# Optimization experiments

Hardware: AMD Instinct MI355X
Metric: run time of the kernel (lower is better)

## Reference

```python
import jax, jax.numpy as jnp
import numpy as np

NUM_HEADS = 16
DIM = 1024
HEAD_DIM = DIM // NUM_HEADS
SCALE = HEAD_DIM ** -0.5


def setup_inputs() -> dict:
    key = jax.random.key(0)
    ks = jax.random.split(key, 6)
    b, n = 2, 1024
    x = jax.random.normal(ks[0], (b, n, DIM), dtype=jnp.float32)
    Wq = jax.random.normal(ks[1], (DIM, DIM), dtype=jnp.float32) * 0.02
    bq = jnp.zeros((DIM,), dtype=jnp.float32)
    Wkv = jax.random.normal(ks[2], (2 * DIM, DIM), dtype=jnp.float32) * 0.02
    bkv = jnp.zeros((2 * DIM,), dtype=jnp.float32)
    Wp = jax.random.normal(ks[3], (DIM, DIM), dtype=jnp.float32) * 0.02
    bp = jnp.zeros((DIM,), dtype=jnp.float32)
    return {"x": x, "Wq": Wq, "bq": bq, "Wkv": Wkv, "bkv": bkv, "Wp": Wp, "bp": bp}


def reference(x, Wq, bq, Wkv, bkv, Wp, bp):
    b, n, c = x.shape
    h, dh = NUM_HEADS, HEAD_DIM
    # self-attention: y = x
    q = (x @ Wq.T + bq).reshape(b, n, h, dh)              # bnhd
    kv = (x @ Wkv.T + bkv).reshape(b, n, 2, h, dh)
    k, v = kv[:, :, 0], kv[:, :, 1]                       # bmhd each
    attn = jnp.einsum('bnhd,bmhd->bnmh', q, k) * SCALE    # bnmh scores
    attn = jax.nn.softmax(attn, axis=2)                   # softmax over m
    out = jnp.einsum('bnmh,bmhd->bnhd', attn, v).reshape(b, n, c)
    out = out @ Wp.T + bp
    return (out, attn)
```

## Files before the change

kernel.cpp:

```cpp
#include <hip/hip_runtime.h>
#include <hip/hip_bf16.h>
#include <stdint.h>


#define NB   2
#define SEQ  1024
#define CDIM 1024
#define NH   16
#define HD   64
#define ROWS (NB*SEQ)
#define ATT_SCALE 0.125f

typedef __attribute__((ext_vector_type(8))) short bf16x8;
typedef __attribute__((ext_vector_type(4))) float f32x4;

#define MFMA16(a,b,c) __builtin_amdgcn_mfma_f32_16x16x32_bf16((a),(b),(c),0,0,0)

static __device__ __forceinline__ unsigned short f2bf(float f) {
  uint32_t x = __builtin_bit_cast(uint32_t, f);
  return (unsigned short)((x + 0x7fffu + ((x >> 16) & 1u)) >> 16);
}
static __device__ __forceinline__ float bf2f(unsigned short u) {
  uint32_t x = ((uint32_t)u) << 16;
  return __builtin_bit_cast(float, x);
}

static __device__ __forceinline__ void gl_lds16(const unsigned short* g,
                                                unsigned short* l) {
  __builtin_amdgcn_global_load_lds(
      (const __attribute__((address_space(1))) unsigned int*)g,
      (__attribute__((address_space(3))) unsigned int*)l,
      16, 0, 0);
}

__global__ __launch_bounds__(256) void k_convert(
    const float* __restrict__ x, const float* __restrict__ Wq,
    const float* __restrict__ Wkv, const float* __restrict__ Wp,
    unsigned short* __restrict__ Xhi, unsigned short* __restrict__ Xlo,
    unsigned short* __restrict__ Whi, unsigned short* __restrict__ Wlo)
{
  const int NX = ROWS * CDIM;
  const int NW = 4096 * CDIM;
  int i = blockIdx.x * 256 + threadIdx.x;
  if (i < NX) {
    float f = x[i];
    unsigned short h = f2bf(f);
    Xhi[i] = h; Xlo[i] = f2bf(f - bf2f(h));
  } else if (i < NX + NW) {
    int w = i - NX;
    int j = w >> 10, c = w & 1023;
    float f = (j < 1024) ? Wq[(size_t)j*1024 + c]
            : (j < 3072) ? Wkv[(size_t)(j-1024)*1024 + c]
                         : Wp[(size_t)(j-3072)*1024 + c];
    unsigned short h = f2bf(f);
    Whi[w] = h; Wlo[w] = f2bf(f - bf2f(h));
  }
}

struct EpiQKV {
  const float* bq; const float* bkv;
  unsigned short *Qhi, *Qlo, *Khi, *Klo, *Vthi, *Vtlo;
  __device__ __forceinline__ void operator()(int m, int n, float v) const {
    if (n < 1024) {
      v += bq[n];
      unsigned short h = f2bf(v);
      size_t o = (size_t)m*1024 + n;
      Qhi[o] = h; Qlo[o] = f2bf(v - bf2f(h));
    } else if (n < 2048) {
      v += bkv[n - 1024];
      size_t o = (size_t)m*1024 + (n - 1024);
      unsigned short h = f2bf(v);
      Khi[o] = h; Klo[o] = f2bf(v - bf2f(h));
    } else {
      v += bkv[n - 1024];
      int c = n - 2048;
      int hh = c >> 6, d = c & 63;
      int b = m >> 10, mm = m & 1023;
      size_t o = ((size_t)((b*NH + hh)*HD + d))*SEQ + mm;
      unsigned short h = f2bf(v);
      Vthi[o] = h; Vtlo[o] = f2bf(v - bf2f(h));
    }
  }
};
struct EpiOut {
  const float* bp; float* out;
  __device__ __forceinline__ void operator()(int m, int n, float v) const {
    out[(size_t)m*1024 + n] = v + bp[n];
  }
};

template <int BM, int BN, class Epi>
__device__ __forceinline__ void gemm_core(
    const unsigned short* __restrict__ Ahi, const unsigned short* __restrict__ Alo, int lda,
    const unsigned short* __restrict__ Bhi, const unsigned short* __restrict__ Blo, int ldb,
    int K, const Epi& epi)
{
  constexpr int FM = BM/32, FN = BN/32;
  constexpr int CA = BM/16, CB = BN/16;
  constexpr int TOT = 2*(CA+CB);
  __shared__ unsigned short sAh[BM*32], sAl[BM*32], sBh[BN*32], sBl[BN*32];
  const int tid  = threadIdx.x;
  const int lane = tid & 63, wave = tid >> 6;
  const int wm = wave & 1, wn = wave >> 1;
  const int bn = blockIdx.x * BN, bm = blockIdx.y * BM;
  const int r = lane & 15, q = lane >> 4;
  const int crow = lane >> 2, ccol = (lane & 3) * 8;

  f32x4 acc[FM][FN];
  #pragma unroll
  for (int i = 0; i < FM; i++)
    #pragma unroll
    for (int j = 0; j < FN; j++) {
      acc[i][j][0]=0.f; acc[i][j][1]=0.f; acc[i][j][2]=0.f; acc[i][j][3]=0.f;
    }

  for (int k0 = 0; k0 < K; k0 += 32) {
    #pragma unroll
    for (int t = 0; t < TOT/4; t++) {
      int c = wave + t*4;
      const unsigned short* gb; unsigned short* sb; int rr, grow, ld;
      if (c < CA)            { gb=Ahi; sb=sAh; rr=c;         grow=bm; ld=lda; }
      else if (c < 2*CA)     { gb=Alo; sb=sAl; rr=c-CA;      grow=bm; ld=lda; }
      else if (c < 2*CA+CB)  { gb=Bhi; sb=sBh; rr=c-2*CA;    grow=bn; ld=ldb; }
      else                   { gb=Blo; sb=sBl; rr=c-2*CA-CB; grow=bn; ld=ldb; }
      int row = rr*16 + crow;
      gl_lds16(gb + (size_t)(grow + row)*ld + k0 + ccol, sb + rr*512);
    }
    __syncthreads();
    bf16x8 ah[FM], al[FM], bh[FN], bl[FN];
    #pragma unroll
    for (int i = 0; i < FM; i++) {
      int oa = (wm*(BM/2) + i*16 + r)*32 + q*8;
      ah[i] = *(const bf16x8*)(sAh + oa);
      al[i] = *(const bf16x8*)(sAl + oa);
    }
    #pragma unroll
    for (int j = 0; j < FN; j++) {
      int ob = (wn*(BN/2) + j*16 + r)*32 + q*8;
      bh[j] = *(const bf16x8*)(sBh + ob);
      bl[j] = *(const bf16x8*)(sBl + ob);
    }
    #pragma unroll
    for (int i = 0; i < FM; i++)
      #pragma unroll
      for (int j = 0; j < FN; j++) {
        acc[i][j] = MFMA16(ah[i], bh[j], acc[i][j]);
        acc[i][j] = MFMA16(ah[i], bl[j], acc[i][j]);
        acc[i][j] = MFMA16(al[i], bh[j], acc[i][j]);
      }
    __syncthreads();
  }
  #pragma unroll
  for (int i = 0; i < FM; i++)
    #pragma unroll
    for (int j = 0; j < FN; j++)
      #pragma unroll
      for (int t = 0; t < 4; t++)
        epi(bm + wm*(BM/2) + i*16 + q*4 + t, bn + wn*(BN/2) + j*16 + r, acc[i][j][t]);
}

__global__ __launch_bounds__(256) void k_gemm_qkv(
    const unsigned short* Xhi, const unsigned short* Xlo,
    const unsigned short* Whi, const unsigned short* Wlo,
    const float* bq, const float* bkv,
    unsigned short* Qhi, unsigned short* Qlo,
    unsigned short* Khi, unsigned short* Klo,
    unsigned short* Vthi, unsigned short* Vtlo)
{
  EpiQKV e{bq, bkv, Qhi, Qlo, Khi, Klo, Vthi, Vtlo};
  gemm_core<128,128>(Xhi, Xlo, CDIM, Whi, Wlo, CDIM, CDIM, e);
}

__global__ __launch_bounds__(256) void k_gemm_out(
    const unsigned short* OAhi, const unsigned short* OAlo,
    const unsigned short* Wphi, const unsigned short* Wplo,
    const float* bp, float* out)
{
  EpiOut e{bp, out};
  gemm_core<64,64>(OAhi, OAlo, CDIM, Wphi, Wplo, CDIM, CDIM, e);
}

#define SLAB_PAD 20
__global__ __launch_bounds__(128) void k_logits(
    const unsigned short* __restrict__ Qhi, const unsigned short* __restrict__ Qlo,
    const unsigned short* __restrict__ Khi, const unsigned short* __restrict__ Klo,
    float* __restrict__ attn)
{
  int mt = blockIdx.x, nt = blockIdx.y, b = blockIdx.z;
  int n0 = nt*16, m0 = mt*32;
  __shared__ unsigned short sQh[16*64], sQl[16*64], sKh[32*64], sKl[32*64];
  __shared__ float slab[16*32*SLAB_PAD];
  const int tid = threadIdx.x, lane = tid & 63, wave = tid >> 6;
  const int r = lane & 15, q = lane >> 4;
  const int crow8 = lane >> 3, ccol8 = (lane & 7) * 8;

  for (int h = 0; h < NH; h++) {
    #pragma unroll
    for (int t = 0; t < 6; t++) {
      int c = wave + t*2;
      const unsigned short* gb; unsigned short* sb; int rr, base;
      if (c < 2)      { gb=Qhi; sb=sQh; rr=c;   base=n0; }
      else if (c < 4) { gb=Qlo; sb=sQl; rr=c-2; base=n0; }
      else if (c < 8) { gb=Khi; sb=sKh; rr=c-4; base=m0; }
      else            { gb=Klo; sb=sKl; rr=c-8; base=m0; }
      int row = rr*8 + crow8;
      gl_lds16(gb + (size_t)(b*SEQ + base + row)*CDIM + h*HD + ccol8, sb + rr*512);
    }
    __syncthreads();
    {
      f32x4 acc; acc[0]=0.f; acc[1]=0.f; acc[2]=0.f; acc[3]=0.f;
      #pragma unroll
      for (int ks = 0; ks < 2; ks++) {
        bf16x8 qh = *(const bf16x8*)(sQh + r*64 + ks*32 + q*8);
        bf16x8 ql = *(const bf16x8*)(sQl + r*64 + ks*32 + q*8);
        bf16x8 kh = *(const bf16x8*)(sKh + (wave*16 + r)*64 + ks*32 + q*8);
        bf16x8 kl = *(const bf16x8*)(sKl + (wave*16 + r)*64 + ks*32 + q*8);
        acc = MFMA16(qh, kh, acc);
        acc = MFMA16(qh, kl, acc);
        acc = MFMA16(ql, kh, acc);
      }
      #pragma unroll
      for (int t = 0; t < 4; t++) {
        int nn = q*4 + t;
        int mm = wave*16 + r;
        slab[(nn*32 + mm)*SLAB_PAD + h] = acc[t] * ATT_SCALE;
      }
    }
    __syncthreads();
  }
  for (int it = 0; it < 16; it++) {
    int idx = it*128 + tid;
    int nn = idx >> 7;
    int rem = idx & 127;
    int flat = rem * 4;
    int mm = flat >> 4, hh = flat & 15;
    float4 v = *(float4*)&slab[(nn*32 + mm)*SLAB_PAD + hh];
    size_t g = (size_t)(b*SEQ + n0 + nn)*(SEQ*NH) + (size_t)(m0 + mm)*NH + hh;
    *(float4*)(attn + g) = v;
  }
}

__global__ __launch_bounds__(256) void k_softmax(
    float* __restrict__ attn, unsigned short* __restrict__ P,
    float* __restrict__ scale_pv)
{
  int n = blockIdx.x, b = blockIdx.y;
  __shared__ float slab[SEQ*NH];
  __shared__ float red[256];
  __shared__ float gmax[16], ginv[16];
  const int tid = threadIdx.x;
  const size_t base = (size_t)(b*SEQ + n) * (SEQ*NH);

  for (int it = 0; it < 16; it++) {
    int f4 = it*256 + tid;
    *(float4*)&slab[f4*4] = *(const float4*)(attn + base + (size_t)f4*4);
  }
  __syncthreads();
  const int h = tid & 15, mq = tid >> 4;
  float mx = -1e30f;
  for (int i = 0; i < 64; i++) mx = fmaxf(mx, slab[(mq*64 + i)*16 + h]);
  red[tid] = mx;
  __syncthreads();
  if (tid < 16) {
    float m2 = red[tid];
    for (int j = 1; j < 16; j++) m2 = fmaxf(m2, red[j*16 + tid]);
    gmax[tid] = m2;
  }
  __syncthreads();
  float gm = gmax[h];
  float s = 0.f;
  for (int i = 0; i < 64; i++) {
    int idx = (mq*64 + i)*16 + h;
    float p = __expf(slab[idx] - gm);
    slab[idx] = p;
    s += p;
  }
  red[tid] = s;
  __syncthreads();
  if (tid < 16) {
    float s2 = 0.f;
    for (int j = 0; j < 16; j++) s2 += red[j*16 + tid];
    float inv = 1.0f / s2;
    ginv[tid] = inv;
    scale_pv[(size_t)(b*SEQ + n)*NH + tid] = inv * (1.0f/65535.0f);
  }
  __syncthreads();
  for (int it = 0; it < 16; it++) {
    int f4 = it*256 + tid;
    int flat = f4*4;
    int hh = flat & 15;
    float4 v = *(float4*)&slab[flat];
    float4 iv = *(float4*)&ginv[hh];
    v.x *= iv.x; v.y *= iv.y; v.z *= iv.z; v.w *= iv.w;
    *(float4*)(attn + base + (size_t)flat) = v;
  }
  int h2 = tid >> 4, l16 = tid & 15;
  size_t pbase = ((size_t)((b*NH + h2)*SEQ + n))*SEQ;
  for (int i = 0; i < 64; i++) {
    int m = i*16 + l16;
    float p = slab[m*16 + h2];
    unsigned int u = (unsigned int)(p * 65535.0f + 0.5f);
    P[pbase + m] = (unsigned short)u;
  }
}

__global__ __launch_bounds__(256) void k_pv(
    const unsigned short* __restrict__ P,
    const unsigned short* __restrict__ Vthi, const unsigned short* __restrict__ Vtlo,
    const float* __restrict__ scale_pv,
    unsigned short* __restrict__ OAhi, unsigned short* __restrict__ OAlo)
{
  int nt = blockIdx.x, h = blockIdx.y, b = blockIdx.z;
  int n0 = nt * 64;
  __shared__ unsigned short sPa[64*32], sPb[64*32], sVh[64*32], sVl[64*32];
  const int tid = threadIdx.x, lane = tid & 63, wave = tid >> 6;
  const int wm = wave & 1, wn = wave >> 1;
  const int r = lane & 15, q = lane >> 4;
  const int crow = lane >> 2, ccol = (lane & 3) * 8;
  const size_t pbase = ((size_t)(b*NH + h))*SEQ*SEQ;
  const size_t vbase = ((size_t)(b*NH + h))*HD*SEQ;

  f32x4 acc[2][2];
  #pragma unroll
  for (int i = 0; i < 2; i++)
    #pragma unroll
    for (int j = 0; j < 2; j++) {
      acc[i][j][0]=0.f; acc[i][j][1]=0.f; acc[i][j][2]=0.f; acc[i][j][3]=0.f;
    }

  for (int k0 = 0; k0 < SEQ; k0 += 32) {
    #pragma unroll
    for (int t = 0; t < 2; t++) {
      int c = wave + t*4;
      const unsigned short* gb = (c < 4) ? Vthi : Vtlo;
      unsigned short* sb = (c < 4) ? (unsigned short*)sVh : (unsigned short*)sVl;
      int rr = c & 3;
      int row = rr*16 + crow;
      gl_lds16(gb + vbase + (size_t)row*SEQ + k0 + ccol, sb + rr*512);
    }
    {
      int row = tid >> 2, ch = (tid & 3) * 8;
      uint4 v = *(const uint4*)(P + pbase + (size_t)(n0 + row)*SEQ + k0 + ch);
      unsigned int wds[4] = {v.x, v.y, v.z, v.w};
      unsigned int pa[4], pb[4];
      #pragma unroll
      for (int e = 0; e < 4; e++) {
        unsigned int lo16 = wds[e] & 0xFFFFu;
        unsigned int hi16 = wds[e] >> 16;
        unsigned int a0 = __builtin_bit_cast(uint32_t, (float)(lo16 & 0xFF00u)) >> 16;
        unsigned int b0 = __builtin_bit_cast(uint32_t, (float)(lo16 & 0x00FFu)) >> 16;
        unsigned int a1 = __builtin_bit_cast(uint32_t, (float)(hi16 & 0xFF00u)) >> 16;
        unsigned int b1 = __builtin_bit_cast(uint32_t, (float)(hi16 & 0x00FFu)) >> 16;
        pa[e] = a0 | (a1 << 16);
        pb[e] = b0 | (b1 << 16);
      }
      *(uint4*)(sPa + row*32 + ch) = make_uint4(pa[0],pa[1],pa[2],pa[3]);
      *(uint4*)(sPb + row*32 + ch) = make_uint4(pb[0],pb[1],pb[2],pb[3]);
    }
    __syncthreads();
    bf16x8 pa[2], pb[2], vh[2], vl[2];
    #pragma unroll
    for (int i = 0; i < 2; i++) {
      int off = (wm*32 + i*16 + r)*32 + q*8;
      pa[i] = *(const bf16x8*)(sPa + off);
      pb[i] = *(const bf16x8*)(sPb + off);
    }
    #pragma unroll
    for (int j = 0; j < 2; j++) {
      int off = (wn*32 + j*16 + r)*32 + q*8;
      vh[j] = *(const bf16x8*)(sVh + off);
      vl[j] = *(const bf16x8*)(sVl + off);
    }
    #pragma unroll
    for (int i = 0; i < 2; i++)
      #pragma unroll
      for (int j = 0; j < 2; j++) {
        acc[i][j] = MFMA16(pa[i], vh[j], acc[i][j]);
        acc[i][j] = MFMA16(pb[i], vh[j], acc[i][j]);
        acc[i][j] = MFMA16(pa[i], vl[j], acc[i][j]);
      }
    __syncthreads();
  }
  #pragma unroll
  for (int i = 0; i < 2; i++)
    #pragma unroll
    for (int t = 0; t < 4; t++) {
      int nn = n0 + wm*32 + i*16 + q*4 + t;
      float sc = scale_pv[(size_t)(b*SEQ + nn)*NH + h];
      #pragma unroll
      for (int j = 0; j < 2; j++) {
        int d = wn*32 + j*16 + r;
        float val = acc[i][j][t] * sc;
        size_t o = (size_t)(b*SEQ + nn)*CDIM + h*HD + d;
        unsigned short hb = f2bf(val);
        OAhi[o] = hb; OAlo[o] = f2bf(val - bf2f(hb));
      }
    }
}

extern "C" void kernel_launch(void* const* d_in, const int* in_sizes, int n_in,
                              void* d_out, int out_size, void* d_ws, size_t ws_size,
                              hipStream_t stream)
{
  const float* x   = (const float*)d_in[0];
  const float* Wq  = (const float*)d_in[1];
  const float* bq  = (const float*)d_in[2];
  const float* Wkv = (const float*)d_in[3];
  const float* bkv = (const float*)d_in[4];
  const float* Wp  = (const float*)d_in[5];
  const float* bp  = (const float*)d_in[6];

  float* out  = (float*)d_out;
  float* attn = out + (size_t)ROWS*CDIM;

  char* w = (char*)d_ws;
  unsigned short* Xhi  = (unsigned short*)w; w += (size_t)ROWS*CDIM*2;
  unsigned short* Xlo  = (unsigned short*)w; w += (size_t)ROWS*CDIM*2;
  unsigned short* Whi  = (unsigned short*)w; w += (size_t)4096*CDIM*2;
  unsigned short* Wlo  = (unsigned short*)w; w += (size_t)4096*CDIM*2;
  unsigned short* Qhi  = (unsigned short*)w; w += (size_t)ROWS*CDIM*2;
  unsigned short* Qlo  = (unsigned short*)w; w += (size_t)ROWS*CDIM*2;
  unsigned short* Khi  = (unsigned short*)w; w += (size_t)ROWS*CDIM*2;
  unsigned short* Klo  = (unsigned short*)w; w += (size_t)ROWS*CDIM*2;
  unsigned short* Vthi = (unsigned short*)w; w += (size_t)NB*NH*HD*SEQ*2;
  unsigned short* Vtlo = (unsigned short*)w; w += (size_t)NB*NH*HD*SEQ*2;
  unsigned short* OAhi = (unsigned short*)w; w += (size_t)ROWS*CDIM*2;
  unsigned short* OAlo = (unsigned short*)w; w += (size_t)ROWS*CDIM*2;
  float* scale_pv      = (float*)w;          w += (size_t)NB*SEQ*NH*4;
  unsigned short* P    = (unsigned short*)w; w += (size_t)NB*NH*SEQ*SEQ*2;

  k_convert<<<dim3((ROWS*CDIM + 4096*CDIM)/256), 256, 0, stream>>>(
      x, Wq, Wkv, Wp, Xhi, Xlo, Whi, Wlo);

  k_gemm_qkv<<<dim3(3072/128, 2048/128), 256, 0, stream>>>(
      Xhi, Xlo, Whi, Wlo, bq, bkv, Qhi, Qlo, Khi, Klo, Vthi, Vtlo);

  k_logits<<<dim3(SEQ/32, SEQ/16, NB), 128, 0, stream>>>(Qhi, Qlo, Khi, Klo, attn);

  k_softmax<<<dim3(SEQ, NB), 256, 0, stream>>>(attn, P, scale_pv);

  k_pv<<<dim3(SEQ/64, NH, NB), 256, 0, stream>>>(P, Vthi, Vtlo, scale_pv, OAhi, OAlo);

  k_gemm_out<<<dim3(1024/64, 2048/64), 256, 0, stream>>>(
      OAhi, OAlo, Whi + (size_t)3072*CDIM, Wlo + (size_t)3072*CDIM, bp, out);
}
```

Measured before the change: 421.9 us.

## Fuse logits and softmax per head group and rebuild attn from quantized P

Merges the logits and softmax kernels into one kernel. Each block computes the full 1024-wide score rows for 16 queries across 8 heads in LDS, using double-buffered, XOR-swizzled K staging, then writes the normalized probabilities straight to the 16-bit P buffer. A separate final kernel expands P back into the fp32 attn output, and the per-row scale buffer is dropped because P is now pre-normalized. This removes the fp32 attn write/read/write round trip, but each block now needs a large LDS allocation and the grid is small. The returned attn is now quantized to 1/65535 steps.

Result: no change. 419.5 us (-0.6%).

```diff
diff --git a/kernel.cpp b/kernel.cpp
--- a/kernel.cpp
+++ b/kernel.cpp
@@ -10,6 +10,7 @@
 #define HD   64
 #define ROWS (NB*SEQ)
 #define ATT_SCALE 0.125f
+#define S23  1028
 
 typedef __attribute__((ext_vector_type(8))) short bf16x8;
 typedef __attribute__((ext_vector_type(4))) float f32x4;
@@ -180,134 +181,162 @@
   gemm_core<64,64>(OAhi, OAlo, CDIM, Wphi, Wplo, CDIM, CDIM, e);
 }
 
-#define SLAB_PAD 20
-__global__ __launch_bounds__(128) void k_logits(
+static __device__ __forceinline__ void stage_q23(
+    const unsigned short* Qhi, const unsigned short* Qlo,
+    size_t qrow0, int col0, unsigned short* sQ,
+    int wave, int drow, int dseg)
+{
+  int p = wave >> 1, t = wave & 1;
+  const unsigned short* g = p ? Qlo : Qhi;
+  gl_lds16(g + (qrow0 + t*8 + drow)*CDIM + col0 + dseg*8,
+           sQ + p*1024 + t*512);
+}
+static __device__ __forceinline__ void stage_k23(
+    const unsigned short* Khi, const unsigned short* Klo,
+    size_t krow0, int col0, unsigned short* dstbuf,
+    int wave, int drow, int dseg)
+{
+  #pragma unroll
+  for (int u = 0; u < 8; u++) {
+    int c = wave*8 + u;
+    int p = c >> 4, t = c & 15;
+    const unsigned short* g = p ? Klo : Khi;
+    gl_lds16(g + (krow0 + t*8 + drow)*CDIM + col0 + dseg*8,
+             dstbuf + p*8192 + t*512);
+  }
+}
+
+__global__ __launch_bounds__(256) void k_logits_softmax(
     const unsigned short* __restrict__ Qhi, const unsigned short* __restrict__ Qlo,
     const unsigned short* __restrict__ Khi, const unsigned short* __restrict__ Klo,
-    float* __restrict__ attn)
-{
-  int mt = blockIdx.x, nt = blockIdx.y, b = blockIdx.z;
-  int n0 = nt*16, m0 = mt*32;
-  __shared__ unsigned short sQh[16*64], sQl[16*64], sKh[32*64], sKl[32*64];
-  __shared__ float slab[16*32*SLAB_PAD];
+    unsigned short* __restrict__ P)
+{
+  const int nt = blockIdx.x, hg = blockIdx.y, b = blockIdx.z;
+  const int n0 = nt*16;
+  __shared__ unsigned short sQ[2*1024];
+  __shared__ unsigned short sK[2][2*8192];
+  __shared__ float slab[16*S23];
+  __shared__ float red[256];
+  __shared__ float gmax[16], gscale[16];
   const int tid = threadIdx.x, lane = tid & 63, wave = tid >> 6;
   const int r = lane & 15, q = lane >> 4;
-  const int crow8 = lane >> 3, ccol8 = (lane & 7) * 8;
-
-  for (int h = 0; h < NH; h++) {
-    #pragma unroll
-    for (int t = 0; t < 6; t++) {
-      int c = wave + t*2;
-      const unsigned short* gb; unsigned short* sb; int rr, base;
-      if (c < 2)      { gb=Qhi; sb=sQh; rr=c;   base=n0; }
-      else if (c < 4) { gb=Qlo; sb=sQl; rr=c-2; base=n0; }
-      else if (c < 8) { gb=Khi; sb=sKh; rr=c-4; base=m0; }
-      else            { gb=Klo; sb=sKl; rr=c-8; base=m0; }
-      int row = rr*8 + crow8;
-      gl_lds16(gb + (size_t)(b*SEQ + base + row)*CDIM + h*HD + ccol8, sb + rr*512);
-    }
-    __syncthreads();
-    {
-      f32x4 acc; acc[0]=0.f; acc[1]=0.f; acc[2]=0.f; acc[3]=0.f;
-      #pragma unroll
-      for (int ks = 0; ks < 2; ks++) {
-        bf16x8 qh = *(const bf16x8*)(sQh + r*64 + ks*32 + q*8);
-        bf16x8 ql = *(const bf16x8*)(sQl + r*64 + ks*32 + q*8);
-        bf16x8 kh = *(const bf16x8*)(sKh + (wave*16 + r)*64 + ks*32 + q*8);
-        bf16x8 kl = *(const bf16x8*)(sKl + (wave*16 + r)*64 + ks*32 + q*8);
-        acc = MFMA16(qh, kh, acc);
-        acc = MFMA16(qh, kl, acc);
-        acc = MFMA16(ql, kh, acc);
+  const int drow = lane >> 3, dseg = (lane & 7) ^ drow;
+  const int sw = r & 7;
+  const size_t qrow0 = (size_t)b*SEQ + n0;
+  const size_t krow0 = (size_t)b*SEQ;
+
+  {
+    int col0 = (hg*8)*HD;
+    stage_q23(Qhi, Qlo, qrow0, col0, sQ, wave, drow, dseg);
+    stage_k23(Khi, Klo, krow0, col0, sK[0], wave, drow, dseg);
+  }
+
+  for (int hh = 0; hh < 8; hh++) {
+    const int h = hg*8 + hh;
+    const int col0 = h*HD;
+    __syncthreads();
+    bf16x8 qh[2], ql[2];
+    #pragma unroll
+    for (int ks = 0; ks < 2; ks++) {
+      int phys = r*64 + (((ks*4 + q) ^ sw))*8;
+      qh[ks] = *(const bf16x8*)(sQ + phys);
+      ql[ks] = *(const bf16x8*)(sQ + 1024 + phys);
+    }
+    for (int c128 = 0; c128 < 8; c128++) {
+      unsigned short* cur = sK[c128 & 1];
+      if (c128 < 7)
+        stage_k23(Khi, Klo, krow0 + (size_t)(c128+1)*128, col0,
+                  sK[(c128+1)&1], wave, drow, dseg);
+      #pragma unroll
+      for (int fr = 0; fr < 2; fr++) {
+        const int mb = wave*32 + fr*16;
+        f32x4 acc; acc[0]=0.f; acc[1]=0.f; acc[2]=0.f; acc[3]=0.f;
+        #pragma unroll
+        for (int ks = 0; ks < 2; ks++) {
+          int phys = (mb + r)*64 + (((ks*4 + q) ^ sw))*8;
+          bf16x8 kh = *(const bf16x8*)(cur + phys);
+          bf16x8 kl = *(const bf16x8*)(cur + 8192 + phys);
+          acc = MFMA16(qh[ks], kh, acc);
+          acc = MFMA16(qh[ks], kl, acc);
+          acc = MFMA16(ql[ks], kh, acc);
+        }
+        #pragma unroll
+        for (int t = 0; t < 4; t++)
+          slab[(q*4+t)*S23 + c128*128 + mb + r] = acc[t] * ATT_SCALE;
       }
-      #pragma unroll
-      for (int t = 0; t < 4; t++) {
-        int nn = q*4 + t;
-        int mm = wave*16 + r;
-        slab[(nn*32 + mm)*SLAB_PAD + h] = acc[t] * ATT_SCALE;
-      }
-    }
-    __syncthreads();
-  }
-  for (int it = 0; it < 16; it++) {
-    int idx = it*128 + tid;
-    int nn = idx >> 7;
-    int rem = idx & 127;
-    int flat = rem * 4;
-    int mm = flat >> 4, hh = flat & 15;
-    float4 v = *(float4*)&slab[(nn*32 + mm)*SLAB_PAD + hh];
-    size_t g = (size_t)(b*SEQ + n0 + nn)*(SEQ*NH) + (size_t)(m0 + mm)*NH + hh;
-    *(float4*)(attn + g) = v;
-  }
-}
-
-__global__ __launch_bounds__(256) void k_softmax(
-    float* __restrict__ attn, unsigned short* __restrict__ P,
-    float* __restrict__ scale_pv)
-{
-  int n = blockIdx.x, b = blockIdx.y;
-  __shared__ float slab[SEQ*NH];
-  __shared__ float red[256];
-  __shared__ float gmax[16], ginv[16];
-  const int tid = threadIdx.x;
-  const size_t base = (size_t)(b*SEQ + n) * (SEQ*NH);
-
-  for (int it = 0; it < 16; it++) {
-    int f4 = it*256 + tid;
-    *(float4*)&slab[f4*4] = *(const float4*)(attn + base + (size_t)f4*4);
-  }
-  __syncthreads();
-  const int h = tid & 15, mq = tid >> 4;
-  float mx = -1e30f;
-  for (int i = 0; i < 64; i++) mx = fmaxf(mx, slab[(mq*64 + i)*16 + h]);
-  red[tid] = mx;
-  __syncthreads();
-  if (tid < 16) {
-    float m2 = red[tid];
-    for (int j = 1; j < 16; j++) m2 = fmaxf(m2, red[j*16 + tid]);
-    gmax[tid] = m2;
-  }
-  __syncthreads();
-  float gm = gmax[h];
-  float s = 0.f;
-  for (int i = 0; i < 64; i++) {
-    int idx = (mq*64 + i)*16 + h;
-    float p = __expf(slab[idx] - gm);
-    slab[idx] = p;
-    s += p;
-  }
-  red[tid] = s;
-  __syncthreads();
-  if (tid < 16) {
-    float s2 = 0.f;
-    for (int j = 0; j < 16; j++) s2 += red[j*16 + tid];
-    float inv = 1.0f / s2;
-    ginv[tid] = inv;
-    scale_pv[(size_t)(b*SEQ + n)*NH + tid] = inv * (1.0f/65535.0f);
-  }
-  __syncthreads();
-  for (int it = 0; it < 16; it++) {
-    int f4 = it*256 + tid;
-    int flat = f4*4;
-    int hh = flat & 15;
-    float4 v = *(float4*)&slab[flat];
-    float4 iv = *(float4*)&ginv[hh];
-    v.x *= iv.x; v.y *= iv.y; v.z *= iv.z; v.w *= iv.w;
-    *(float4*)(attn + base + (size_t)flat) = v;
-  }
-  int h2 = tid >> 4, l16 = tid & 15;
-  size_t pbase = ((size_t)((b*NH + h2)*SEQ + n))*SEQ;
-  for (int i = 0; i < 64; i++) {
-    int m = i*16 + l16;
-    float p = slab[m*16 + h2];
-    unsigned int u = (unsigned int)(p * 65535.0f + 0.5f);
-    P[pbase + m] = (unsigned short)u;
-  }
+      __syncthreads();
+    }
+    if (hh < 7) {
+      int ncol = (h+1)*HD;
+      stage_q23(Qhi, Qlo, qrow0, ncol, sQ, wave, drow, dseg);
+      stage_k23(Khi, Klo, krow0, ncol, sK[0], wave, drow, dseg);
+    }
+    const int n = tid >> 4, c = tid & 15;
+    float mx = -1e30f;
+    #pragma unroll 8
+    for (int j = 0; j < 64; j++)
+      mx = fmaxf(mx, slab[n*S23 + c + j*16]);
+    red[tid] = mx;
+    __syncthreads();
+    if (tid < 16) {
+      float m2 = red[tid*16];
+      for (int j = 1; j < 16; j++) m2 = fmaxf(m2, red[tid*16 + j]);
+      gmax[tid] = m2;
+    }
+    __syncthreads();
+    const float gm = gmax[n];
+    float s = 0.f;
+    #pragma unroll 8
+    for (int j = 0; j < 64; j++) {
+      int idx = n*S23 + c + j*16;
+      float p = __expf(slab[idx] - gm);
+      slab[idx] = p;
+      s += p;
+    }
+    red[tid] = s;
+    __syncthreads();
+    if (tid < 16) {
+      float s2 = 0.f;
+      for (int j = 0; j < 16; j++) s2 += red[tid*16 + j];
+      gscale[tid] = 65535.0f / s2;
+    }
+    __syncthreads();
+    const float sc = gscale[n];
+    const size_t pb = ((size_t)((b*NH + h)*SEQ) + n0 + n)*SEQ;
+    #pragma unroll
+    for (int j = 0; j < 8; j++) {
+      int m0 = (j*16 + c)*8;
+      float4 v0 = *(const float4*)&slab[n*S23 + m0];
+      float4 v1 = *(const float4*)&slab[n*S23 + m0 + 4];
+      unsigned int u0 = (unsigned)(v0.x*sc + 0.5f) | ((unsigned)(v0.y*sc + 0.5f) << 16);
+      unsigned int u1 = (unsigned)(v0.z*sc + 0.5f) | ((unsigned)(v0.w*sc + 0.5f) << 16);
+      unsigned int u2 = (unsigned)(v1.x*sc + 0.5f) | ((unsigned)(v1.y*sc + 0.5f) << 16);
+      unsigned int u3 = (unsigned)(v1.z*sc + 0.5f) | ((unsigned)(v1.w*sc + 0.5f) << 16);
+      *(uint4*)(P + pb + m0) = make_uint4(u0, u1, u2, u3);
+    }
+  }
+}
+
+__global__ __launch_bounds__(256) void k_attn_write(
+    const unsigned short* __restrict__ P, float* __restrict__ attn)
+{
+  int T = blockIdx.x*256 + threadIdx.x;
+  int b = T >> 20, rem = T & 1048575;
+  int n = rem >> 10, m = rem & 1023;
+  const size_t pb = ((size_t)(b*NH)*SEQ + n)*SEQ + m;
+  float v[16];
+  #pragma unroll
+  for (int h = 0; h < 16; h++)
+    v[h] = (float)P[pb + (size_t)h*SEQ*SEQ] * (1.0f/65535.0f);
+  size_t ob = ((size_t)(b*SEQ + n)*SEQ + m)*16;
+  #pragma unroll
+  for (int g = 0; g < 4; g++)
+    *(float4*)(attn + ob + g*4) = make_float4(v[g*4], v[g*4+1], v[g*4+2], v[g*4+3]);
 }
 
 __global__ __launch_bounds__(256) void k_pv(
     const unsigned short* __restrict__ P,
     const unsigned short* __restrict__ Vthi, const unsigned short* __restrict__ Vtlo,
-    const float* __restrict__ scale_pv,
     unsigned short* __restrict__ OAhi, unsigned short* __restrict__ OAlo)
 {
   int nt = blockIdx.x, h = blockIdx.y, b = blockIdx.z;
@@ -342,7 +371,7 @@
       int row = tid >> 2, ch = (tid & 3) * 8;
       uint4 v = *(const uint4*)(P + pbase + (size_t)(n0 + row)*SEQ + k0 + ch);
       unsigned int wds[4] = {v.x, v.y, v.z, v.w};
-      unsigned int pa[4], pb[4];
+      unsigned int pa[4], pb4[4];
       #pragma unroll
       for (int e = 0; e < 4; e++) {
         unsigned int lo16 = wds[e] & 0xFFFFu;
@@ -351,19 +380,19 @@
         unsigned int b0 = __builtin_bit_cast(uint32_t, (float)(lo16 & 0x00FFu)) >> 16;
         unsigned int a1 = __builtin_bit_cast(uint32_t, (float)(hi16 & 0xFF00u)) >> 16;
         unsigned int b1 = __builtin_bit_cast(uint32_t, (float)(hi16 & 0x00FFu)) >> 16;
-        pa[e] = a0 | (a1 << 16);
-        pb[e] = b0 | (b1 << 16);
+        pa[e]  = a0 | (a1 << 16);
+        pb4[e] = b0 | (b1 << 16);
       }
       *(uint4*)(sPa + row*32 + ch) = make_uint4(pa[0],pa[1],pa[2],pa[3]);
-      *(uint4*)(sPb + row*32 + ch) = make_uint4(pb[0],pb[1],pb[2],pb[3]);
-    }
-    __syncthreads();
-    bf16x8 pa[2], pb[2], vh[2], vl[2];
+      *(uint4*)(sPb + row*32 + ch) = make_uint4(pb4[0],pb4[1],pb4[2],pb4[3]);
+    }
+    __syncthreads();
+    bf16x8 pa[2], pb2[2], vh[2], vl[2];
     #pragma unroll
     for (int i = 0; i < 2; i++) {
       int off = (wm*32 + i*16 + r)*32 + q*8;
-      pa[i] = *(const bf16x8*)(sPa + off);
-      pb[i] = *(const bf16x8*)(sPb + off);
+      pa[i]  = *(const bf16x8*)(sPa + off);
+      pb2[i] = *(const bf16x8*)(sPb + off);
     }
     #pragma unroll
     for (int j = 0; j < 2; j++) {
@@ -375,9 +404,9 @@
     for (int i = 0; i < 2; i++)
       #pragma unroll
       for (int j = 0; j < 2; j++) {
-        acc[i][j] = MFMA16(pa[i], vh[j], acc[i][j]);
-        acc[i][j] = MFMA16(pb[i], vh[j], acc[i][j]);
-        acc[i][j] = MFMA16(pa[i], vl[j], acc[i][j]);
+        acc[i][j] = MFMA16(pa[i],  vh[j], acc[i][j]);
+        acc[i][j] = MFMA16(pb2[i], vh[j], acc[i][j]);
+        acc[i][j] = MFMA16(pa[i],  vl[j], acc[i][j]);
       }
     __syncthreads();
   }
@@ -386,11 +415,10 @@
     #pragma unroll
     for (int t = 0; t < 4; t++) {
       int nn = n0 + wm*32 + i*16 + q*4 + t;
-      float sc = scale_pv[(size_t)(b*SEQ + nn)*NH + h];
       #pragma unroll
       for (int j = 0; j < 2; j++) {
         int d = wn*32 + j*16 + r;
-        float val = acc[i][j][t] * sc;
+        float val = acc[i][j][t] * (1.0f/65535.0f);
         size_t o = (size_t)(b*SEQ + nn)*CDIM + h*HD + d;
         unsigned short hb = f2bf(val);
         OAhi[o] = hb; OAlo[o] = f2bf(val - bf2f(hb));
@@ -426,7 +454,6 @@
   unsigned short* Vtlo = (unsigned short*)w; w += (size_t)NB*NH*HD*SEQ*2;
   unsigned short* OAhi = (unsigned short*)w; w += (size_t)ROWS*CDIM*2;
   unsigned short* OAlo = (unsigned short*)w; w += (size_t)ROWS*CDIM*2;
-  float* scale_pv      = (float*)w;          w += (size_t)NB*SEQ*NH*4;
   unsigned short* P    = (unsigned short*)w; w += (size_t)NB*NH*SEQ*SEQ*2;
 
   k_convert<<<dim3((ROWS*CDIM + 4096*CDIM)/256), 256, 0, stream>>>(
@@ -435,12 +462,13 @@
   k_gemm_qkv<<<dim3(3072/128, 2048/128), 256, 0, stream>>>(
       Xhi, Xlo, Whi, Wlo, bq, bkv, Qhi, Qlo, Khi, Klo, Vthi, Vtlo);
 
-  k_logits<<<dim3(SEQ/32, SEQ/16, NB), 128, 0, stream>>>(Qhi, Qlo, Khi, Klo, attn);
-
-  k_softmax<<<dim3(SEQ, NB), 256, 0, stream>>>(attn, P, scale_pv);
-
-  k_pv<<<dim3(SEQ/64, NH, NB), 256, 0, stream>>>(P, Vthi, Vtlo, scale_pv, OAhi, OAlo);
+  k_logits_softmax<<<dim3(SEQ/16, 2, NB), 256, 0, stream>>>(
+      Qhi, Qlo, Khi, Klo, P);
+
+  k_pv<<<dim3(SEQ/64, NH, NB), 256, 0, stream>>>(P, Vthi, Vtlo, OAhi, OAlo);
 
   k_gemm_out<<<dim3(1024/64, 2048/64), 256, 0, stream>>>(
       OAhi, OAlo, Whi + (size_t)3072*CDIM, Wlo + (size_t)3072*CDIM, bp, out);
-}
+
+  k_attn_write<<<dim3((NB*SEQ*SEQ)/256), 256, 0, stream>>>(P, attn);
+}
```
